# Kernel optimization log

Measured on AMD Instinct MI355X. Metric: run time of the kernel, lower is better.

## Reference

```python
import jax, jax.numpy as jnp
import numpy as np

L, T, F = 16, 262144, 2
N = 524288
HIDDEN, OUT = 64, 3
_b = np.exp((np.log(64.0) - np.log(16.0)) / (L - 1))
# per-level resolutions: floor(N_min * b**l), kept as float for the scale multiply
N_VALUES = np.floor(np.float32(16.0 * _b ** np.arange(L))).astype(np.float32)


def setup_inputs() -> dict:
    key = jax.random.key(0)
    ks = jax.random.split(key, 6)
    X = jax.random.uniform(ks[0], (N, 2), jnp.float32)
    hash_table = jax.random.uniform(ks[1], (L, T, F), jnp.float32, minval=-1e-4, maxval=1e-4)

    def lin(k, fan_in, fan_out):
        kw, kb = jax.random.split(k)
        bound = 1.0 / np.sqrt(fan_in)
        W = jax.random.uniform(kw, (fan_in, fan_out), jnp.float32, minval=-bound, maxval=bound)
        b = jax.random.uniform(kb, (fan_out,), jnp.float32, minval=-bound, maxval=bound)
        return W, b

    W1, b1 = lin(ks[2], L * F, HIDDEN)
    W2, b2 = lin(ks[3], HIDDEN, HIDDEN)
    W3, b3 = lin(ks[4], HIDDEN, HIDDEN)
    W4, b4 = lin(ks[5], HIDDEN, OUT)
    return dict(X=X, hash_table=hash_table, W1=W1, b1=b1, W2=W2, b2=b2,
                W3=W3, b3=b3, W4=W4, b4=b4)


def _encode(X, hash_table):
    nvals = jnp.asarray(N_VALUES)
    x_scaled = X[:, :, None] * nvals                      # [N,2,L]
    frac = x_scaled - jnp.floor(x_scaled)                 # [N,2,L]
    vertices = jnp.array([[0., 0., 1., 1.], [0., 1., 0., 1.]], jnp.float32)  # [2,4]
    # faithful to source: scaled coord * vertex mask (not floor + offset), then int truncation
    x_vert = (x_scaled[:, :, :, None] * vertices[None, :, None, :]).astype(jnp.uint32)  # [N,2,L,4]
    primes = jnp.array([1, 2654435761], dtype=jnp.uint32)
    xt = x_vert * primes[None, :, None, None]
    # source takes xor then mod 2 (not mod T); LSB is exact under uint32 wraparound
    x_hash = (jnp.bitwise_xor(xt[:, 0], xt[:, 1]) % 2).astype(jnp.int32)  # [N,L,4] in {0,1}
    xp = jnp.transpose(x_hash, (1, 0, 2))                 # [L,N,4]
    # faithful to source's torch.gather along dim 0: out[l,n,k,f] = table[hash, k, f]
    lookup = hash_table[xp, jnp.arange(4)[None, None, :], :]  # [L,N,4,F]
    lookup = jnp.transpose(lookup, (1, 0, 2, 3))          # [N,L,4,F]
    fx, fy = frac[:, 0, :], frac[:, 1, :]
    cx, cy = 1.0 - fx, 1.0 - fy
    f_stack = jnp.stack([cx * cy, cx * fy, fx * cy, fx * fy], axis=2)  # [N,L,4]
    x_interp = jnp.einsum('nlv,nlvf->nlf', f_stack, lookup)           # [N,L,F]
    return x_interp.reshape(-1, L * F)


def reference(X, hash_table, W1, b1, W2, b2, W3, b3, W4, b4):
    h = _encode(X, hash_table)
    lrelu = lambda z: jnp.where(z >= 0, z, 0.01 * z)  # LeakyReLU default slope
    h = lrelu(h @ W1 + b1)
    h = lrelu(h @ W2 + b2)
    h = lrelu(h @ W3 + b3)
    return jax.nn.relu(h @ W4 + b4)
```

## Files before the change

### kernel.cpp

```cpp
#include <hip/hip_runtime.h>


typedef float  f32x4  __attribute__((ext_vector_type(4)));
typedef __bf16 bf16x4 __attribute__((ext_vector_type(4)));
typedef __bf16 bf16x8 __attribute__((ext_vector_type(8)));

#define MFMA16(A, B, C) __builtin_amdgcn_mfma_f32_16x16x32_bf16((A), (B), (C), 0, 0, 0)

__global__ __launch_bounds__(256) void hashnerf_mfma(
    const float* __restrict__ X,
    const float* __restrict__ HT,
    const float* __restrict__ W1, const float* __restrict__ B1,
    const float* __restrict__ W2, const float* __restrict__ B2,
    const float* __restrict__ W3, const float* __restrict__ B3,
    const float* __restrict__ W4, const float* __restrict__ B4,
    float* __restrict__ out, int npts)
{
    __shared__ __align__(16) float  sBias[208];
    __shared__ __align__(16) __bf16 sHh[4][16 * 72];
    __shared__ __align__(16) __bf16 sHl[4][16 * 72];

    const int tid = threadIdx.x;
    if (tid < 64) {
        sBias[tid]       = B1[tid];
        sBias[64 + tid]  = B2[tid];
        sBias[128 + tid] = B3[tid];
    }
    if (tid < 16) sBias[192 + tid] = (tid < 3) ? B4[tid] : 0.0f;
    __syncthreads();

    const int l  = tid & 63;
    const int p  = l & 15;
    const int g  = l >> 4;
    const int wv = tid >> 6;
    __bf16* __restrict__ Hh = sHh[wv];
    __bf16* __restrict__ Hl = sHl[wv];

    bf16x8 w1h[4];
#pragma unroll
    for (int t = 0; t < 4; ++t)
#pragma unroll
        for (int e = 0; e < 8; ++e)
            w1h[t][e] = (__bf16)W1[(8 * g + e) * 64 + p + 16 * t];

    bf16x8 w2h[4][2], w2l[4][2], w3h[4][2], w3l[4][2];
#pragma unroll
    for (int t = 0; t < 4; ++t)
#pragma unroll
        for (int s = 0; s < 2; ++s)
#pragma unroll
            for (int e = 0; e < 8; ++e) {
                float w2 = W2[(32 * s + 8 * g + e) * 64 + p + 16 * t];
                __bf16 h2 = (__bf16)w2;
                w2h[t][s][e] = h2; w2l[t][s][e] = (__bf16)(w2 - (float)h2);
                float w3 = W3[(32 * s + 8 * g + e) * 64 + p + 16 * t];
                __bf16 h3 = (__bf16)w3;
                w3h[t][s][e] = h3; w3l[t][s][e] = (__bf16)(w3 - (float)h3);
            }

    bf16x8 w4h[2], w4l[2];
#pragma unroll
    for (int s = 0; s < 2; ++s)
#pragma unroll
        for (int e = 0; e < 8; ++e) {
            float w = (p < 3) ? W4[(32 * s + 8 * g + e) * 3 + p] : 0.0f;
            __bf16 h = (__bf16)w;
            w4h[s][e] = h; w4l[s][e] = (__bf16)(w - (float)h);
        }

    float t0[8], t1[8];
#pragma unroll
    for (int e = 0; e < 8; ++e) { t0[e] = HT[e]; t1[e] = HT[524288 + e]; }

    const float NVA[4] = {16.f, 17.f, 19.f, 21.f};
    const float NVB[4] = {23.f, 25.f, 27.f, 30.f};
    const float NVC[4] = {33.f, 36.f, 40.f, 44.f};
    const float NVD[4] = {48.f, 53.f, 58.f, 64.f};
    float nv4[4];
#pragma unroll
    for (int j = 0; j < 4; ++j)
        nv4[j] = (g == 0) ? NVA[j] : (g == 1) ? NVB[j] : (g == 2) ? NVC[j] : NVD[j];

    auto mlp_layer = [&](const bf16x8 (&wh)[4][2], const bf16x8 (&wl)[4][2],
                         const float* __restrict__ bofs) {
        f32x4 a2[4];
#pragma unroll
        for (int t = 0; t < 4; ++t)
            a2[t] = *reinterpret_cast<const f32x4*>(&bofs[16 * t + 4 * g]);
#pragma unroll
        for (int s = 0; s < 2; ++s) {
            bf16x8 xh = *reinterpret_cast<const bf16x8*>(&Hh[p * 72 + 32 * s + 8 * g]);
            bf16x8 xl = *reinterpret_cast<const bf16x8*>(&Hl[p * 72 + 32 * s + 8 * g]);
#pragma unroll
            for (int t = 0; t < 4; ++t) {
                a2[t] = MFMA16(wh[t][s], xh, a2[t]);
                a2[t] = MFMA16(wh[t][s], xl, a2[t]);
                a2[t] = MFMA16(wl[t][s], xh, a2[t]);
            }
        }
#pragma unroll
        for (int t = 0; t < 4; ++t) {
            f32x4 v = a2[t];
            bf16x4 hv, lv;
#pragma unroll
            for (int r = 0; r < 4; ++r) {
                v[r] = fmaxf(v[r], 0.01f * v[r]);
                __bf16 h = (__bf16)v[r];
                hv[r] = h;
                lv[r] = (__bf16)(v[r] - (float)h);
            }
            *reinterpret_cast<bf16x4*>(&Hh[p * 72 + 16 * t + 4 * g]) = hv;
            *reinterpret_cast<bf16x4*>(&Hl[p * 72 + 16 * t + 4 * g]) = lv;
        }
    };

    const int wave_global = blockIdx.x * 4 + wv;
    const int nwaves = gridDim.x * 4;
    const int ntiles = (npts + 15) >> 4;
    const float2* X2 = reinterpret_cast<const float2*>(X);

    int tile = wave_global;
    float2 xv = make_float2(0.f, 0.f);
    if (tile < ntiles) xv = X2[min(tile * 16 + p, npts - 1)];

    for (; tile < ntiles; tile += nwaves) {
        const int nt = tile + nwaves;
        float2 xnext = xv;
        if (nt < ntiles) xnext = X2[min(nt * 16 + p, npts - 1)];

        bf16x8 bh;
#pragma unroll
        for (int j2 = 0; j2 < 4; ++j2) {
            const float nv = nv4[j2];
            const float sx = xv.x * nv, sy = xv.y * nv;
            const float fx = sx - floorf(sx), fy = sy - floorf(sy);
            const unsigned ix = (unsigned)sx, iy = (unsigned)sy;
            const bool px = (ix & 1u) != 0u, py = (iy & 1u) != 0u;
            const bool pz = px != py;
            const float cx = 1.f - fx, cy = 1.f - fy;
            const float q0 = cx * cy, q1 = cx * fy, q2 = fx * cy, q3 = fx * fy;
            float a0 = q0 * t0[0];
            a0 = fmaf(q1, py ? t1[2] : t0[2], a0);
            a0 = fmaf(q2, px ? t1[4] : t0[4], a0);
            a0 = fmaf(q3, pz ? t1[6] : t0[6], a0);
            float a1 = q0 * t0[1];
            a1 = fmaf(q1, py ? t1[3] : t0[3], a1);
            a1 = fmaf(q2, px ? t1[5] : t0[5], a1);
            a1 = fmaf(q3, pz ? t1[7] : t0[7], a1);
            bh[2 * j2]     = (__bf16)a0;
            bh[2 * j2 + 1] = (__bf16)a1;
        }

        f32x4 acc[4];
#pragma unroll
        for (int t = 0; t < 4; ++t) {
            acc[t] = *reinterpret_cast<const f32x4*>(&sBias[16 * t + 4 * g]);
            acc[t] = MFMA16(w1h[t], bh, acc[t]);
        }
#pragma unroll
        for (int t = 0; t < 4; ++t) {
            f32x4 v = acc[t];
            bf16x4 hv, lv;
#pragma unroll
            for (int r = 0; r < 4; ++r) {
                v[r] = fmaxf(v[r], 0.01f * v[r]);
                __bf16 h = (__bf16)v[r];
                hv[r] = h;
                lv[r] = (__bf16)(v[r] - (float)h);
            }
            *reinterpret_cast<bf16x4*>(&Hh[p * 72 + 16 * t + 4 * g]) = hv;
            *reinterpret_cast<bf16x4*>(&Hl[p * 72 + 16 * t + 4 * g]) = lv;
        }

        mlp_layer(w2h, w2l, &sBias[64]);
        mlp_layer(w3h, w3l, &sBias[128]);

        f32x4 ao = *reinterpret_cast<const f32x4*>(&sBias[192 + 4 * g]);
#pragma unroll
        for (int s = 0; s < 2; ++s) {
            bf16x8 xh = *reinterpret_cast<const bf16x8*>(&Hh[p * 72 + 32 * s + 8 * g]);
            bf16x8 xl = *reinterpret_cast<const bf16x8*>(&Hl[p * 72 + 32 * s + 8 * g]);
            ao = MFMA16(w4h[s], xh, ao);
            ao = MFMA16(w4h[s], xl, ao);
            ao = MFMA16(w4l[s], xh, ao);
        }
        if (g == 0 && tile * 16 + p < npts) {
            float* op = out + (size_t)(tile * 16 + p) * 3;
            op[0] = fmaxf(ao[0], 0.0f);
            op[1] = fmaxf(ao[1], 0.0f);
            op[2] = fmaxf(ao[2], 0.0f);
        }

        xv = xnext;
    }
}

extern "C" void kernel_launch(void* const* d_in, const int* in_sizes, int n_in,
                              void* d_out, int out_size, void* d_ws, size_t ws_size,
                              hipStream_t stream) {
    const float* X  = (const float*)d_in[0];
    const float* HT = (const float*)d_in[1];
    const float* W1 = (const float*)d_in[2];
    const float* B1 = (const float*)d_in[3];
    const float* W2 = (const float*)d_in[4];
    const float* B2 = (const float*)d_in[5];
    const float* W3 = (const float*)d_in[6];
    const float* B3 = (const float*)d_in[7];
    const float* W4 = (const float*)d_in[8];
    const float* B4 = (const float*)d_in[9];
    float* out = (float*)d_out;

    const int npts = in_sizes[0] / 2;
    hipLaunchKernelGGL(hashnerf_mfma, dim3(768), dim3(256), 0, stream,
                       X, HT, W1, B1, W2, B2, W3, B3, W4, B4, out, npts);
}
```

Measured before the change: 155.9 us.

## Interleave two point tiles per wave to hide MFMA dependency latency

Each wave now processes two 16-point tiles per loop iteration. Their MFMA chains for every layer are interleaved, so independent accumulators can hide the MFMA dependency latency that a single serial accumulator chain exposes. Shared-memory activation buffers are doubled per wave and the row stride is changed from 72 to 88 to alter the LDS bank mapping. The grid shrinks from 768 to 512 blocks. In exchange, register pressure and LDS use go up, which may lower occupancy.

```diff
diff --git a/kernel.cpp b/kernel.cpp
--- a/kernel.cpp
+++ b/kernel.cpp
@@ -6,6 +6,8 @@
 typedef __bf16 bf16x8 __attribute__((ext_vector_type(8)));
 
 #define MFMA16(A, B, C) __builtin_amdgcn_mfma_f32_16x16x32_bf16((A), (B), (C), 0, 0, 0)
+
+#define HSTRIDE 88
 
 __global__ __launch_bounds__(256) void hashnerf_mfma(
     const float* __restrict__ X,
@@ -17,8 +19,8 @@
     float* __restrict__ out, int npts)
 {
     __shared__ __align__(16) float  sBias[208];
-    __shared__ __align__(16) __bf16 sHh[4][16 * 72];
-    __shared__ __align__(16) __bf16 sHl[4][16 * 72];
+    __shared__ __align__(16) __bf16 sHh[4][2][16 * HSTRIDE];
+    __shared__ __align__(16) __bf16 sHl[4][2][16 * HSTRIDE];
 
     const int tid = threadIdx.x;
     if (tid < 64) {
@@ -33,8 +35,10 @@
     const int p  = l & 15;
     const int g  = l >> 4;
     const int wv = tid >> 6;
-    __bf16* __restrict__ Hh = sHh[wv];
-    __bf16* __restrict__ Hl = sHl[wv];
+    __bf16* __restrict__ HhA = sHh[wv][0];
+    __bf16* __restrict__ HlA = sHl[wv][0];
+    __bf16* __restrict__ HhB = sHh[wv][1];
+    __bf16* __restrict__ HlB = sHl[wv][1];
 
     bf16x8 w1h[4];
 #pragma unroll
@@ -81,53 +85,7 @@
     for (int j = 0; j < 4; ++j)
         nv4[j] = (g == 0) ? NVA[j] : (g == 1) ? NVB[j] : (g == 2) ? NVC[j] : NVD[j];
 
-    auto mlp_layer = [&](const bf16x8 (&wh)[4][2], const bf16x8 (&wl)[4][2],
-                         const float* __restrict__ bofs) {
-        f32x4 a2[4];
-#pragma unroll
-        for (int t = 0; t < 4; ++t)
-            a2[t] = *reinterpret_cast<const f32x4*>(&bofs[16 * t + 4 * g]);
-#pragma unroll
-        for (int s = 0; s < 2; ++s) {
-            bf16x8 xh = *reinterpret_cast<const bf16x8*>(&Hh[p * 72 + 32 * s + 8 * g]);
-            bf16x8 xl = *reinterpret_cast<const bf16x8*>(&Hl[p * 72 + 32 * s + 8 * g]);
-#pragma unroll
-            for (int t = 0; t < 4; ++t) {
-                a2[t] = MFMA16(wh[t][s], xh, a2[t]);
-                a2[t] = MFMA16(wh[t][s], xl, a2[t]);
-                a2[t] = MFMA16(wl[t][s], xh, a2[t]);
-            }
-        }
-#pragma unroll
-        for (int t = 0; t < 4; ++t) {
-            f32x4 v = a2[t];
-            bf16x4 hv, lv;
-#pragma unroll
-            for (int r = 0; r < 4; ++r) {
-                v[r] = fmaxf(v[r], 0.01f * v[r]);
-                __bf16 h = (__bf16)v[r];
-                hv[r] = h;
-                lv[r] = (__bf16)(v[r] - (float)h);
-            }
-            *reinterpret_cast<bf16x4*>(&Hh[p * 72 + 16 * t + 4 * g]) = hv;
-            *reinterpret_cast<bf16x4*>(&Hl[p * 72 + 16 * t + 4 * g]) = lv;
-        }
-    };
-
-    const int wave_global = blockIdx.x * 4 + wv;
-    const int nwaves = gridDim.x * 4;
-    const int ntiles = (npts + 15) >> 4;
-    const float2* X2 = reinterpret_cast<const float2*>(X);
-
-    int tile = wave_global;
-    float2 xv = make_float2(0.f, 0.f);
-    if (tile < ntiles) xv = X2[min(tile * 16 + p, npts - 1)];
-
-    for (; tile < ntiles; tile += nwaves) {
-        const int nt = tile + nwaves;
-        float2 xnext = xv;
-        if (nt < ntiles) xnext = X2[min(nt * 16 + p, npts - 1)];
-
+    auto encode = [&](float2 xv) -> bf16x8 {
         bf16x8 bh;
 #pragma unroll
         for (int j2 = 0; j2 < 4; ++j2) {
@@ -150,16 +108,14 @@
             bh[2 * j2]     = (__bf16)a0;
             bh[2 * j2 + 1] = (__bf16)a1;
         }
-
-        f32x4 acc[4];
+        return bh;
+    };
+
+    auto split_store = [&](f32x4 (&a2)[4], __bf16* __restrict__ Hh_,
+                           __bf16* __restrict__ Hl_) {
 #pragma unroll
         for (int t = 0; t < 4; ++t) {
-            acc[t] = *reinterpret_cast<const f32x4*>(&sBias[16 * t + 4 * g]);
-            acc[t] = MFMA16(w1h[t], bh, acc[t]);
-        }
-#pragma unroll
-        for (int t = 0; t < 4; ++t) {
-            f32x4 v = acc[t];
+            f32x4 v = a2[t];
             bf16x4 hv, lv;
 #pragma unroll
             for (int r = 0; r < 4; ++r) {
@@ -168,30 +124,103 @@
                 hv[r] = h;
                 lv[r] = (__bf16)(v[r] - (float)h);
             }
-            *reinterpret_cast<bf16x4*>(&Hh[p * 72 + 16 * t + 4 * g]) = hv;
-            *reinterpret_cast<bf16x4*>(&Hl[p * 72 + 16 * t + 4 * g]) = lv;
-        }
-
-        mlp_layer(w2h, w2l, &sBias[64]);
-        mlp_layer(w3h, w3l, &sBias[128]);
-
-        f32x4 ao = *reinterpret_cast<const f32x4*>(&sBias[192 + 4 * g]);
+            *reinterpret_cast<bf16x4*>(&Hh_[p * HSTRIDE + 16 * t + 4 * g]) = hv;
+            *reinterpret_cast<bf16x4*>(&Hl_[p * HSTRIDE + 16 * t + 4 * g]) = lv;
+        }
+    };
+
+    auto layer_pair = [&](const bf16x8 (&wh)[4][2], const bf16x8 (&wl)[4][2],
+                          const float* __restrict__ bofs) {
+        f32x4 aA[4], aB[4];
+#pragma unroll
+        for (int t = 0; t < 4; ++t) {
+            aA[t] = *reinterpret_cast<const f32x4*>(&bofs[16 * t + 4 * g]);
+            aB[t] = aA[t];
+        }
 #pragma unroll
         for (int s = 0; s < 2; ++s) {
-            bf16x8 xh = *reinterpret_cast<const bf16x8*>(&Hh[p * 72 + 32 * s + 8 * g]);
-            bf16x8 xl = *reinterpret_cast<const bf16x8*>(&Hl[p * 72 + 32 * s + 8 * g]);
-            ao = MFMA16(w4h[s], xh, ao);
-            ao = MFMA16(w4h[s], xl, ao);
-            ao = MFMA16(w4l[s], xh, ao);
-        }
-        if (g == 0 && tile * 16 + p < npts) {
-            float* op = out + (size_t)(tile * 16 + p) * 3;
-            op[0] = fmaxf(ao[0], 0.0f);
-            op[1] = fmaxf(ao[1], 0.0f);
-            op[2] = fmaxf(ao[2], 0.0f);
-        }
-
-        xv = xnext;
+            bf16x8 xhA = *reinterpret_cast<const bf16x8*>(&HhA[p * HSTRIDE + 32 * s + 8 * g]);
+            bf16x8 xlA = *reinterpret_cast<const bf16x8*>(&HlA[p * HSTRIDE + 32 * s + 8 * g]);
+            bf16x8 xhB = *reinterpret_cast<const bf16x8*>(&HhB[p * HSTRIDE + 32 * s + 8 * g]);
+            bf16x8 xlB = *reinterpret_cast<const bf16x8*>(&HlB[p * HSTRIDE + 32 * s + 8 * g]);
+#pragma unroll
+            for (int t = 0; t < 4; ++t) {
+                aA[t] = MFMA16(wh[t][s], xhA, aA[t]);
+                aB[t] = MFMA16(wh[t][s], xhB, aB[t]);
+                aA[t] = MFMA16(wh[t][s], xlA, aA[t]);
+                aB[t] = MFMA16(wh[t][s], xlB, aB[t]);
+                aA[t] = MFMA16(wl[t][s], xhA, aA[t]);
+                aB[t] = MFMA16(wl[t][s], xhB, aB[t]);
+            }
+        }
+        split_store(aA, HhA, HlA);
+        split_store(aB, HhB, HlB);
+    };
+
+    const int wave_global = blockIdx.x * 4 + wv;
+    const int nw = gridDim.x * 4;
+    const int ntiles = (npts + 15) >> 4;
+    const float2* X2 = reinterpret_cast<const float2*>(X);
+
+    int tA = wave_global;
+    int tB = wave_global + nw;
+    float2 xA = make_float2(0.f, 0.f), xB = xA;
+    if (tA < ntiles) xA = X2[min(tA * 16 + p, npts - 1)];
+    if (tB < ntiles) xB = X2[min(tB * 16 + p, npts - 1)];
+
+    for (; tA < ntiles; tA += 2 * nw, tB += 2 * nw) {
+        const int nA = tA + 2 * nw, nB = tB + 2 * nw;
+        float2 xnA = xA, xnB = xB;
+        if (nA < ntiles) xnA = X2[min(nA * 16 + p, npts - 1)];
+        if (nB < ntiles) xnB = X2[min(nB * 16 + p, npts - 1)];
+        const bool hasB = (tB < ntiles);
+
+        bf16x8 bhA = encode(xA);
+        bf16x8 bhB = encode(xB);
+
+        f32x4 aA[4], aB[4];
+#pragma unroll
+        for (int t = 0; t < 4; ++t) {
+            aA[t] = *reinterpret_cast<const f32x4*>(&sBias[16 * t + 4 * g]);
+            aB[t] = aA[t];
+            aA[t] = MFMA16(w1h[t], bhA, aA[t]);
+            aB[t] = MFMA16(w1h[t], bhB, aB[t]);
+        }
+        split_store(aA, HhA, HlA);
+        split_store(aB, HhB, HlB);
+
+        layer_pair(w2h, w2l, &sBias[64]);
+        layer_pair(w3h, w3l, &sBias[128]);
+
+        f32x4 oA = *reinterpret_cast<const f32x4*>(&sBias[192 + 4 * g]);
+        f32x4 oB = oA;
+#pragma unroll
+        for (int s = 0; s < 2; ++s) {
+            bf16x8 xhA = *reinterpret_cast<const bf16x8*>(&HhA[p * HSTRIDE + 32 * s + 8 * g]);
+            bf16x8 xlA = *reinterpret_cast<const bf16x8*>(&HlA[p * HSTRIDE + 32 * s + 8 * g]);
+            bf16x8 xhB = *reinterpret_cast<const bf16x8*>(&HhB[p * HSTRIDE + 32 * s + 8 * g]);
+            bf16x8 xlB = *reinterpret_cast<const bf16x8*>(&HlB[p * HSTRIDE + 32 * s + 8 * g]);
+            oA = MFMA16(w4h[s], xhA, oA);
+            oB = MFMA16(w4h[s], xhB, oB);
+            oA = MFMA16(w4h[s], xlA, oA);
+            oB = MFMA16(w4h[s], xlB, oB);
+            oA = MFMA16(w4l[s], xhA, oA);
+            oB = MFMA16(w4l[s], xhB, oB);
+        }
+        if (g == 0 && tA * 16 + p < npts) {
+            float* op = out + (size_t)(tA * 16 + p) * 3;
+            op[0] = fmaxf(oA[0], 0.0f);
+            op[1] = fmaxf(oA[1], 0.0f);
+            op[2] = fmaxf(oA[2], 0.0f);
+        }
+        if (g == 0 && hasB && tB * 16 + p < npts) {
+            float* op = out + (size_t)(tB * 16 + p) * 3;
+            op[0] = fmaxf(oB[0], 0.0f);
+            op[1] = fmaxf(oB[1], 0.0f);
+            op[2] = fmaxf(oB[2], 0.0f);
+        }
+
+        xA = xnA; xB = xnB;
     }
 }
 
@@ -211,6 +240,6 @@
     float* out = (float*)d_out;
 
     const int npts = in_sizes[0] / 2;
-    hipLaunchKernelGGL(hashnerf_mfma, dim3(768), dim3(256), 0, stream,
+    hipLaunchKernelGGL(hashnerf_mfma, dim3(512), dim3(256), 0, stream,
                        X, HT, W1, B1, W2, B2, W3, B3, W4, B4, out, npts);
 }
```

New measurement: 153.4 us. About the same (-1.6%).
